# Performance work log

Hardware: AMD Instinct MI355X
Metric: run time of the kernel (lower is better)

The kernel has to match this reference:

```python
import jax, jax.numpy as jnp
import numpy as np

NODE_NUM = 2000
D_MODEL = 2048
IN_DIM = 7
OUT_DIM = 1
NODE_DIM = 40
CONV_CH = 64
SKIP_CH = 64
DEPTH = 3
ALPHA = 0.05
BATCH = 64
KERNEL = D_MODEL - NODE_NUM + 1  # 49
LN_EPS = 1e-5


def setup_inputs() -> dict:
    key = jax.random.key(0)
    ks = jax.random.split(key, 12)
    s = 0.02
    return {
        "x": jax.random.normal(ks[0], (BATCH, IN_DIM * D_MODEL), dtype=jnp.float32),
        "nodevec1": jax.random.normal(ks[1], (NODE_NUM, NODE_DIM), dtype=jnp.float32),
        "nodevec2": jax.random.normal(ks[2], (NODE_DIM, NODE_NUM), dtype=jnp.float32),
        "w_start": jax.random.normal(ks[3], (CONV_CH, IN_DIM, KERNEL), dtype=jnp.float32) * s,
        "b_start": jnp.zeros((CONV_CH,), dtype=jnp.float32),
        "w_mlp": jax.random.normal(ks[4], (SKIP_CH, (DEPTH + 1) * CONV_CH), dtype=jnp.float32) * s,
        "b_mlp": jnp.zeros((SKIP_CH,), dtype=jnp.float32),
        "w_end": jax.random.normal(ks[5], (OUT_DIM, SKIP_CH), dtype=jnp.float32) * s,
        "b_end": jnp.zeros((OUT_DIM,), dtype=jnp.float32),
        "w_lin": jax.random.normal(ks[6], (D_MODEL, NODE_NUM), dtype=jnp.float32) * s,
        "b_lin": jnp.zeros((D_MODEL,), dtype=jnp.float32),
        "ln_g": jnp.ones((D_MODEL,), dtype=jnp.float32),
        "ln_b": jnp.zeros((D_MODEL,), dtype=jnp.float32),
    }


def _conv1d(x, w, b):
    # x: (B, Cin, L), w: (Cout, Cin, K) -> (B, Cout, L-K+1)
    y = jax.lax.conv_general_dilated(x, w, window_strides=(1,), padding='VALID',
                                     dimension_numbers=('NCH', 'OIH', 'NCH'))
    return y + b[None, :, None]


def _layernorm(x, g, b):
    mu = jnp.mean(x, axis=-1, keepdims=True)
    var = jnp.mean(jnp.square(x - mu), axis=-1, keepdims=True)
    return (x - mu) * jax.lax.rsqrt(var + LN_EPS) * g + b


def reference(x, nodevec1, nodevec2, w_start, b_start, w_mlp, b_mlp,
              w_end, b_end, w_lin, b_lin, ln_g, ln_b):
    # adaptive adjacency: softmax(relu(E1 @ E2), axis=1)
    adp = jax.nn.softmax(jax.nn.relu(nodevec1 @ nodevec2), axis=1)  # (N, N)

    out = x.reshape(x.shape[0], IN_DIM, D_MODEL)
    out = _conv1d(out, w_start, b_start)  # (B, CONV_CH, N)

    # mixprop
    adj = adp + jnp.eye(NODE_NUM, dtype=adp.dtype)
    a = adj / jnp.sum(adj, axis=1, keepdims=True)  # row-normalized (N, N)
    h = out
    hops = [h]
    for _ in range(DEPTH):
        # einsum('ncw,vw->ncv', h, a)
        h = ALPHA * out + (1.0 - ALPHA) * jnp.einsum('bcw,vw->bcv', h, a)
        hops.append(h)
    ho = jnp.concatenate(hops, axis=1)  # (B, (DEPTH+1)*CONV_CH, N)
    ho = jnp.einsum('bcn,oc->bon', ho, w_mlp) + b_mlp[None, :, None]  # 1x1 conv

    out = jax.nn.gelu(ho, approximate=False)
    out = jnp.einsum('bcn,oc->bon', out, w_end) + b_end[None, :, None]  # (B, 1, N)
    out = jnp.squeeze(out, axis=1)  # (B, N)
    out = out @ w_lin.T + b_lin  # (B, D_MODEL)
    out = _layernorm(out, ln_g, ln_b)
    return out.reshape(out.shape[0], -1)
```

## Files before the change

### kernel.cpp

```cpp
#include <hip/hip_runtime.h>

#define NODE_NUM 2000
#define DM 2048
#define IN_DIM 7
#define CONV_CH 64
#define KER 49
#define BATCH 64

typedef __attribute__((ext_vector_type(8))) short bf16x8;
typedef __attribute__((ext_vector_type(4))) float f32x4;
typedef __attribute__((ext_vector_type(4))) unsigned int u32x4;

__device__ __forceinline__ float bf2f(unsigned short u) {
  union { unsigned int i; float f; } c; c.i = ((unsigned int)u) << 16; return c.f;
}
__device__ __forceinline__ unsigned short f2bf(float f) {
  union { float f; unsigned int i; } c; c.f = f;
  unsigned int r = c.i + 0x7FFFu + ((c.i >> 16) & 1u);
  return (unsigned short)(r >> 16);
}

__global__ __launch_bounds__(256) void adj_kernel(const float* __restrict__ nv1,
                                                  const float* __restrict__ nv2,
                                                  unsigned short* __restrict__ Ab) {
  const int bid = blockIdx.x;
  const int tid = threadIdx.x;
  if (bid >= 500) {
    const int r0 = 2000 + (bid - 500) * 4;
    for (int i = tid; i < 4 * 2048; i += 256)
      Ab[(size_t)(r0 + (i >> 11)) * DM + (i & 2047)] = 0;
    return;
  }
  const int v0 = bid * 4;
  __shared__ float e1s[4][40];
  __shared__ float redm[4][4], redsum[4][4];
  for (int i = tid; i < 160; i += 256) e1s[i / 40][i % 40] = nv1[(v0 + i / 40) * 40 + i % 40];
  __syncthreads();
  const int w0 = tid * 8;
  const bool oob = (w0 >= NODE_NUM);
  const float* base = nv2 + (oob ? 0 : w0);
  float acc[4][8] = {};
  f32x4 xa = *(const f32x4*)(base);
  f32x4 xb = *(const f32x4*)(base + 4);
  for (int k = 0; k < 40; ++k) {
    const f32x4 ca = xa, cb = xb;
    if (k < 39) {
      xa = *(const f32x4*)(base + (k + 1) * NODE_NUM);
      xb = *(const f32x4*)(base + (k + 1) * NODE_NUM + 4);
    }
#pragma unroll
    for (int v = 0; v < 4; ++v) {
      const float e = e1s[v][k];
#pragma unroll
      for (int i = 0; i < 4; ++i) {
        acc[v][i]     = fmaf(e, ca[i], acc[v][i]);
        acc[v][i + 4] = fmaf(e, cb[i], acc[v][i + 4]);
      }
    }
  }
  const int wid = tid >> 6, lane = tid & 63;
#pragma unroll
  for (int v = 0; v < 4; ++v) {
    float mx = -1e30f;
    if (!oob) {
#pragma unroll
      for (int i = 0; i < 8; ++i) {
        acc[v][i] = fmaxf(acc[v][i], 0.f);
        mx = fmaxf(mx, acc[v][i]);
      }
    }
    for (int o = 32; o; o >>= 1) mx = fmaxf(mx, __shfl_xor(mx, o));
    if (lane == 0) redm[v][wid] = mx;
  }
  __syncthreads();
#pragma unroll
  for (int v = 0; v < 4; ++v) {
    const float mx = fmaxf(fmaxf(redm[v][0], redm[v][1]), fmaxf(redm[v][2], redm[v][3]));
    float sum = 0.f;
    if (!oob) {
#pragma unroll
      for (int i = 0; i < 8; ++i) { const float e = __expf(acc[v][i] - mx); acc[v][i] = e; sum += e; }
    }
    for (int o = 32; o; o >>= 1) sum += __shfl_xor(sum, o);
    if (lane == 0) redsum[v][wid] = sum;
  }
  __syncthreads();
#pragma unroll
  for (int v = 0; v < 4; ++v) {
    const float sum = redsum[v][0] + redsum[v][1] + redsum[v][2] + redsum[v][3];
    const float inv = 0.5f / sum;
    const int vg = v0 + v;
    unsigned short out[8];
#pragma unroll
    for (int i = 0; i < 8; ++i) {
      const float val = oob ? 0.f : (acc[v][i] * inv + ((w0 + i == vg) ? 0.5f : 0.f));
      out[i] = f2bf(val);
    }
    *(u32x4*)(Ab + (size_t)vg * DM + w0) = *(const u32x4*)out;
  }
}

__global__ __launch_bounds__(256) void wpack_kernel(const float* __restrict__ wst,
                                                    unsigned short* __restrict__ wpack) {
  const int idx = blockIdx.x * 256 + threadIdx.x;
  const int e = idx & 7;
  const int lane = (idx >> 3) & 63;
  const int w = (idx >> 9) & 3;
  const int kstep = idx >> 11;
  const int c = w * 16 + (lane & 15);
  const int k = kstep * 32 + (lane >> 4) * 8 + e;
  const int ci = k >> 6, kern = k & 63;
  const float val = (kern < KER) ? wst[(c * IN_DIM + ci) * KER + kern] : 0.f;
  wpack[idx] = f2bf(val);
}

__global__ __launch_bounds__(256) void wmpack_kernel(const float* __restrict__ wm,
                                                     unsigned short* __restrict__ wmb) {
  const int idx = blockIdx.x * 256 + threadIdx.x;
  wmb[idx] = f2bf(wm[idx]);
}

__global__ __launch_bounds__(256) void conv_kernel(const float* __restrict__ x,
                                                   const unsigned short* __restrict__ wpack,
                                                   const float* __restrict__ bst,
                                                   unsigned short* __restrict__ H0) {
  __shared__ alignas(16) unsigned short xcopy[8 * 7 * 128];
  const int b = blockIdx.y;
  const int n0 = blockIdx.x * 64;
  const int tid = threadIdx.x;
  const int wv = tid >> 6, lane = tid & 63;
  const int l15 = lane & 15, kg = lane >> 4;
  bf16x8 af[14];
#pragma unroll
  for (int ks = 0; ks < 14; ++ks)
    af[ks] = *(const bf16x8*)(wpack + ((size_t)(ks * 4 + wv) * 64 + lane) * 8);
  f32x4 acc[4];
  {
    const f32x4 bv = *(const f32x4*)(bst + wv * 16 + kg * 4);
#pragma unroll
    for (int nf = 0; nf < 4; ++nf) acc[nf] = bv;
  }
  const size_t xb = (size_t)b * (IN_DIM * DM);
#pragma unroll
  for (int it = 0; it < 14; ++it) {
    const int row = it * 4 + (tid >> 6);
    const int s = row / 7, ci = row % 7;
    const int j = (tid & 63) * 2;
    int g0 = n0 + j + s;     if (g0 > DM - 1) g0 = DM - 1;
    int g1 = n0 + j + 1 + s; if (g1 > DM - 1) g1 = DM - 1;
    const float v0 = x[xb + ci * DM + g0];
    const float v1 = x[xb + ci * DM + g1];
    const unsigned int pk = (unsigned int)f2bf(v0) | ((unsigned int)f2bf(v1) << 16);
    *(unsigned int*)((char*)xcopy + row * 256 + j * 2) = pk;
  }
  __syncthreads();
#pragma unroll
  for (int ks = 0; ks < 14; ++ks) {
    const int ci = ks >> 1;
    const int kern0 = ((ks & 1) << 5) + kg * 8;
#pragma unroll
    for (int nf = 0; nf < 4; ++nf) {
      const int q = nf * 16 + l15 + kern0;
      const int byte = ((q & 7) * 7 + ci) * 256 + (q & ~7) * 2;
      const bf16x8 bfr = *(const bf16x8*)((const char*)xcopy + byte);
      acc[nf] = __builtin_amdgcn_mfma_f32_16x16x32_bf16(af[ks], bfr, acc[nf], 0, 0, 0);
    }
  }
#pragma unroll
  for (int nf = 0; nf < 4; ++nf) {
#pragma unroll
    for (int r = 0; r < 4; ++r) {
      const int c = wv * 16 + kg * 4 + r;
      const int n = n0 + nf * 16 + l15;
      H0[(size_t)(b * 64 + c) * DM + n] =
          (n < NODE_NUM) ? f2bf(acc[nf][r]) : (unsigned short)0;
    }
  }
}

template <int MODE>
__global__ __launch_bounds__(256) void gemm_nt(const unsigned short* __restrict__ A,
                                               const unsigned short* __restrict__ Bt,
                                               const unsigned short* __restrict__ H0,
                                               void* __restrict__ Cout) {
  __shared__ alignas(16) unsigned short As[2][128 * 64];
  __shared__ alignas(16) unsigned short Bs[2][128 * 64];
  const int tid = threadIdx.x;
  int bx, by;
  if (MODE == 0) {
    const int lin = blockIdx.y * 16 + blockIdx.x;
    const int swz = (lin & 7) * 64 + (lin >> 3);
    bx = swz & 15;  by = swz >> 4;
  } else {
    bx = blockIdx.x;  by = blockIdx.y;
  }
  const int n0 = bx * 128;
  const int m0 = (MODE == 0) ? by * 128 : 0;
  const int kbeg = (MODE == 0) ? 0 : by * 256;
  const int nt = (MODE == 0) ? (DM / 64) : 4;
  const int wid = tid >> 6, lane = tid & 63;
  const int wr = wid >> 1, wc = wid & 1;
  const int l15 = lane & 15, kg = lane >> 4;

  auto STAGE = [&](int buf, int k0) {
#pragma unroll
    for (int it = 0; it < 4; ++it) {
      const int lin = it * 4096 + tid * 16;
      const int row = lin >> 7;
      const int blog = (lin & 127) ^ ((row & 7) << 4);
      const char* sa = (const char*)A + ((size_t)(m0 + row) * DM + k0) * 2 + blog;
      const char* sb = (const char*)Bt + ((size_t)(n0 + row) * DM + k0) * 2 + blog;
      __builtin_amdgcn_global_load_lds((const __attribute__((address_space(1))) void*)sa,
                                       (__attribute__((address_space(3))) void*)((char*)As[buf] + lin),
                                       16, 0, 0);
      __builtin_amdgcn_global_load_lds((const __attribute__((address_space(1))) void*)sb,
                                       (__attribute__((address_space(3))) void*)((char*)Bs[buf] + lin),
                                       16, 0, 0);
    }
  };

  f32x4 acc[4][4] = {};
  STAGE(0, kbeg);
  STAGE(1, kbeg + 64);

  for (int t = 0; t < nt; ++t) {
    const int cur = t & 1;
    if (t + 1 < nt) asm volatile("s_waitcnt vmcnt(8)" ::: "memory");
    else            asm volatile("s_waitcnt vmcnt(0)" ::: "memory");
    __builtin_amdgcn_s_barrier();
    __builtin_amdgcn_sched_barrier(0);
    bf16x8 af[2][4], bfr[2][4];
#pragma unroll
    for (int f = 0; f < 4; ++f) {
      const int ra = wr * 64 + f * 16 + l15;
      const int rb = wc * 64 + f * 16 + l15;
#pragma unroll
      for (int kk = 0; kk < 2; ++kk) {
        const int off = kk * 64 + kg * 16;
        af[kk][f]  = *(const bf16x8*)((const char*)As[cur] + ra * 128 + (off ^ ((ra & 7) << 4)));
        bfr[kk][f] = *(const bf16x8*)((const char*)Bs[cur] + rb * 128 + (off ^ ((rb & 7) << 4)));
      }
    }
    asm volatile("s_waitcnt lgkmcnt(0)" ::: "memory");
    __builtin_amdgcn_sched_barrier(0);
    __builtin_amdgcn_s_barrier();
    __builtin_amdgcn_sched_barrier(0);
    if (t + 2 < nt) STAGE(cur, kbeg + (t + 2) * 64);
#pragma unroll
    for (int kk = 0; kk < 2; ++kk)
#pragma unroll
      for (int mf = 0; mf < 4; ++mf)
#pragma unroll
        for (int nf = 0; nf < 4; ++nf)
          acc[mf][nf] = __builtin_amdgcn_mfma_f32_16x16x32_bf16(af[kk][mf], bfr[kk][nf],
                                                                acc[mf][nf], 0, 0, 0);
  }
  const int l4 = lane >> 4;
#pragma unroll
  for (int mf = 0; mf < 4; ++mf) {
#pragma unroll
    for (int nf = 0; nf < 4; ++nf) {
#pragma unroll
      for (int r = 0; r < 4; ++r) {
        const int gm = m0 + wr * 64 + mf * 16 + l4 * 4 + r;
        const int gn = n0 + wc * 64 + nf * 16 + l15;
        if (MODE == 0) {
          const float v = 0.05f * bf2f(H0[(size_t)gm * DM + gn]) + 0.95f * acc[mf][nf][r];
          ((unsigned short*)Cout)[(size_t)gm * DM + gn] = f2bf(v);
        } else {
          if (gm < 64)
            ((float*)Cout)[(size_t)blockIdx.y * 64 * DM + (size_t)gm * DM + gn] = acc[mf][nf][r];
        }
      }
    }
  }
}

__global__ __launch_bounds__(256) void mlp_kernel(const unsigned short* __restrict__ h0,
                                                  const unsigned short* __restrict__ h1,
                                                  const unsigned short* __restrict__ h2,
                                                  const unsigned short* __restrict__ h3,
                                                  const unsigned short* __restrict__ wmb,
                                                  const float* __restrict__ bm,
                                                  const float* __restrict__ we,
                                                  const float* __restrict__ be,
                                                  unsigned short* __restrict__ out1) {
  __shared__ alignas(16) unsigned short hs[64 * 264];
  __shared__ alignas(16) unsigned short wl[64 * 264];
  __shared__ float cbuf[128];
  const int b = blockIdx.y;
  const int gn0 = blockIdx.x * 64;
  const int tid = threadIdx.x;
#pragma unroll
  for (int it = 0; it < 8; ++it) {
    const int idx = it * 256 + tid;
    const int o = idx >> 5, c = (idx & 31) * 8;
    *(bf16x8*)&wl[o * 264 + c] = *(const bf16x8*)(wmb + o * 256 + c);
  }
  if (tid < 64) cbuf[tid] = bm[tid];
  else if (tid < 128) cbuf[tid] = we[tid - 64];
  char* hsb = (char*)hs;
#pragma unroll
  for (int it = 0; it < 8; ++it) {
    const int idx = it * 256 + tid;
    const int cf = idx >> 3, n0 = (idx & 7) * 8;
    const int hop = cf >> 6, c = cf & 63;
    const unsigned short* hb = (hop == 0) ? h0 : (hop == 1) ? h1 : (hop == 2) ? h2 : h3;
    const unsigned long long* p =
        (const unsigned long long*)(hb + (size_t)(b * 64 + c) * DM + gn0 + n0);
    const unsigned long long lo = p[0], hi = p[1];
#pragma unroll
    for (int t = 0; t < 8; ++t) {
      const int i = (t + tid) & 7;
      const unsigned short val = (unsigned short)(((i & 4) ? hi : lo) >> ((i & 3) * 16));
      *(unsigned short*)(hsb + (n0 + i) * 528 + cf * 2) = val;
    }
  }
  __syncthreads();
  const int wid = tid >> 6, lane = tid & 63;
  const int l15 = lane & 15, kg = lane >> 4;
  const char* wb = (const char*)wl;
  f32x4 acc[4] = {};
#pragma unroll
  for (int kk = 0; kk < 8; ++kk) {
    const int koff = kk * 64 + kg * 16;
    const bf16x8 bfr = *(const bf16x8*)(hsb + (wid * 16 + l15) * 528 + koff);
#pragma unroll
    for (int mf = 0; mf < 4; ++mf) {
      const bf16x8 af = *(const bf16x8*)(wb + (mf * 16 + l15) * 528 + koff);
      acc[mf] = __builtin_amdgcn_mfma_f32_16x16x32_bf16(af, bfr, acc[mf], 0, 0, 0);
    }
  }
  float pl = 0.f;
#pragma unroll
  for (int mf = 0; mf < 4; ++mf) {
#pragma unroll
    for (int r = 0; r < 4; ++r) {
      const int o = mf * 16 + kg * 4 + r;
      const float s = acc[mf][r] + cbuf[o];
      const float g = 0.5f * s * (1.f + erff(s * 0.70710678118f));
      pl += cbuf[64 + o] * g;
    }
  }
  pl += __shfl_xor(pl, 16);
  pl += __shfl_xor(pl, 32);
  if (kg == 0) {
    const int n = gn0 + wid * 16 + l15;
    out1[(size_t)b * DM + n] = (n < NODE_NUM) ? f2bf(pl + be[0]) : (unsigned short)0;
  }
}

__global__ __launch_bounds__(256) void wlin_cvt(const float* __restrict__ wlin,
                                                unsigned short* __restrict__ wl) {
  const int idx = (blockIdx.x * 256 + threadIdx.x) * 8;
  const int d = idx >> 11, w0 = idx & 2047;
  unsigned short out[8];
#pragma unroll
  for (int j = 0; j < 8; ++j) {
    const int w = w0 + j;
    out[j] = (w < NODE_NUM) ? f2bf(wlin[d * NODE_NUM + w]) : (unsigned short)0;
  }
  *(u32x4*)(wl + idx) = *(const u32x4*)out;
}

__global__ __launch_bounds__(256) void ln_kernel(const float* __restrict__ yp,
                                                 const float* __restrict__ bl,
                                                 const float* __restrict__ g,
                                                 const float* __restrict__ bb,
                                                 float* __restrict__ out) {
  const int b = blockIdx.x, tid = threadIdx.x;
  __shared__ float rs[4], rq[4];
  float v[8];
  float s = 0.f;
#pragma unroll
  for (int i = 0; i < 8; ++i) {
    const int d = i * 256 + tid;
    float acc = bl[d];
#pragma unroll
    for (int sp = 0; sp < 8; ++sp) acc += yp[(size_t)sp * 64 * DM + (size_t)b * DM + d];
    v[i] = acc;
    s += acc;
  }
  for (int o = 32; o; o >>= 1) s += __shfl_xor(s, o);
  const int wid = tid >> 6, lane = tid & 63;
  if (lane == 0) rs[wid] = s;
  __syncthreads();
  s = rs[0] + rs[1] + rs[2] + rs[3];
  const float mu = s * (1.f / 2048.f);
  float q = 0.f;
#pragma unroll
  for (int i = 0; i < 8; ++i) { const float d = v[i] - mu; q += d * d; }
  for (int o = 32; o; o >>= 1) q += __shfl_xor(q, o);
  if (lane == 0) rq[wid] = q;
  __syncthreads();
  q = rq[0] + rq[1] + rq[2] + rq[3];
  const float inv = rsqrtf(q * (1.f / 2048.f) + 1e-5f);
#pragma unroll
  for (int i = 0; i < 8; ++i) {
    const int d = i * 256 + tid;
    out[(size_t)b * DM + d] = (v[i] - mu) * inv * g[d] + bb[d];
  }
}

extern "C" void kernel_launch(void* const* d_in, const int* in_sizes, int n_in,
                              void* d_out, int out_size, void* d_ws, size_t ws_size,
                              hipStream_t stream) {
  const float* x      = (const float*)d_in[0];
  const float* nv1    = (const float*)d_in[1];
  const float* nv2    = (const float*)d_in[2];
  const float* w_st   = (const float*)d_in[3];
  const float* b_st   = (const float*)d_in[4];
  const float* w_mlp  = (const float*)d_in[5];
  const float* b_mlp  = (const float*)d_in[6];
  const float* w_end  = (const float*)d_in[7];
  const float* b_end  = (const float*)d_in[8];
  const float* w_lin  = (const float*)d_in[9];
  const float* b_lin  = (const float*)d_in[10];
  const float* ln_g   = (const float*)d_in[11];
  const float* ln_b   = (const float*)d_in[12];

  char* ws = (char*)d_ws;
  const size_t SZ_A = (size_t)DM * DM * 2;
  const size_t SZ_H = (size_t)4096 * DM * 2;
  unsigned short* Ab    = (unsigned short*)(ws);
  unsigned short* H0    = (unsigned short*)(ws + SZ_A);
  unsigned short* H1    = (unsigned short*)(ws + SZ_A + SZ_H);
  unsigned short* H2    = (unsigned short*)(ws + SZ_A + 2 * SZ_H);
  unsigned short* H3    = (unsigned short*)(ws + SZ_A + 3 * SZ_H);
  unsigned short* OUT1  = (unsigned short*)(ws + SZ_A + 4 * SZ_H);
  unsigned short* WPACK = (unsigned short*)(ws + SZ_A + 4 * SZ_H + 262144);
  unsigned short* WMB   = (unsigned short*)(ws + SZ_A + 4 * SZ_H + 319488);
  unsigned short* WL    = (unsigned short*)(ws + SZ_A + 4 * SZ_H + 524288);
  float*          YP    = (float*)(ws + SZ_A + 4 * SZ_H + 524288 + SZ_A);

  wpack_kernel<<<112, 256, 0, stream>>>(w_st, WPACK);
  wmpack_kernel<<<64, 256, 0, stream>>>(w_mlp, WMB);
  adj_kernel<<<512, 256, 0, stream>>>(nv1, nv2, Ab);
  conv_kernel<<<dim3(32, BATCH), 256, 0, stream>>>(x, WPACK, b_st, H0);
  wlin_cvt<<<2048, 256, 0, stream>>>(w_lin, WL);

  gemm_nt<0><<<dim3(16, 32), 256, 0, stream>>>(H0, Ab, H0, (void*)H1);
  gemm_nt<0><<<dim3(16, 32), 256, 0, stream>>>(H1, Ab, H0, (void*)H2);
  gemm_nt<0><<<dim3(16, 32), 256, 0, stream>>>(H2, Ab, H0, (void*)H3);

  mlp_kernel<<<dim3(32, BATCH), 256, 0, stream>>>(H0, H1, H2, H3, WMB, b_mlp,
                                                  w_end, b_end, OUT1);
  gemm_nt<1><<<dim3(16, 8), 256, 0, stream>>>(OUT1, WL, (const unsigned short*)0, (void*)YP);
  ln_kernel<<<BATCH, 256, 0, stream>>>(YP, b_lin, ln_g, ln_b, (float*)d_out);
}
```

Before: 263.7 us.

## Use 256x128 tile GEMM with 512 threads and interleaved prefetch for mixprop hops

Replaces the 128x128-tile, 256-thread mixprop GEMM with a 256x128-tile, 8-wave kernel. Next-tile global-to-LDS loads are spread across the MFMA phases, and MFMA issue priority is raised. This raises reuse of the shared adjacency tile and overlaps loads with compute. The grid shrinks from 512 to 256 blocks and LDS use rises, which could lower occupancy and leave CUs idle on a 256-CU part. The tail GEMM is split into its own non-templated kernel.

```diff
diff --git a/kernel.cpp b/kernel.cpp
--- a/kernel.cpp
+++ b/kernel.cpp
@@ -178,26 +178,119 @@
   }
 }
 
-template <int MODE>
-__global__ __launch_bounds__(256) void gemm_nt(const unsigned short* __restrict__ A,
+__global__ __launch_bounds__(512) void gemm256(const unsigned short* __restrict__ A,
                                                const unsigned short* __restrict__ Bt,
                                                const unsigned short* __restrict__ H0,
-                                               void* __restrict__ Cout) {
+                                               unsigned short* __restrict__ C) {
+  __shared__ alignas(16) unsigned short As[2][256 * 64];
+  __shared__ alignas(16) unsigned short Bs[2][128 * 64];
+  const int tid = threadIdx.x;
+  const int lin = blockIdx.y * 16 + blockIdx.x;
+  const int swz = (lin & 7) * 32 + (lin >> 3);
+  const int bx = swz & 15, by = swz >> 4;
+  const int n0 = bx * 128, m0 = by * 256;
+  const int wid = tid >> 6, lane = tid & 63;
+  const int wr = wid >> 2, wc = wid & 3;
+  const int l15 = lane & 15, kg = lane >> 4;
+
+  auto stageA = [&](int buf, int k0, int it) {
+    const int linb = it * 8192 + tid * 16;
+    const int row = linb >> 7;
+    const int blog = (linb & 127) ^ ((row & 7) << 4);
+    const char* s = (const char*)A + ((size_t)(m0 + row) * DM + k0) * 2 + blog;
+    __builtin_amdgcn_global_load_lds((const __attribute__((address_space(1))) void*)s,
+        (__attribute__((address_space(3))) void*)((char*)As[buf] + linb), 16, 0, 0);
+  };
+  auto stageB = [&](int buf, int k0, int it) {
+    const int linb = it * 8192 + tid * 16;
+    const int row = linb >> 7;
+    const int blog = (linb & 127) ^ ((row & 7) << 4);
+    const char* s = (const char*)Bt + ((size_t)(n0 + row) * DM + k0) * 2 + blog;
+    __builtin_amdgcn_global_load_lds((const __attribute__((address_space(1))) void*)s,
+        (__attribute__((address_space(3))) void*)((char*)Bs[buf] + linb), 16, 0, 0);
+  };
+
+  f32x4 acc[8][2] = {};
+  stageA(0, 0, 0); stageA(0, 0, 1); stageA(0, 0, 2); stageA(0, 0, 3);
+  stageB(0, 0, 0); stageB(0, 0, 1);
+
+  for (int t = 0; t < 32; ++t) {
+    const int cur = t & 1, nxt = cur ^ 1;
+    const int kn = (t + 1) * 64;
+    const bool pf = (t + 1 < 32);
+    asm volatile("s_waitcnt vmcnt(0)" ::: "memory");
+    __builtin_amdgcn_s_barrier();
+    __builtin_amdgcn_sched_barrier(0);
+    bf16x8 bfrag[2][2];
+#pragma unroll
+    for (int p = 0; p < 4; ++p) {
+      bf16x8 afr[2][2];
+#pragma unroll
+      for (int ml = 0; ml < 2; ++ml) {
+        const int ra = wr * 128 + (p * 2 + ml) * 16 + l15;
+        const int rowoff = ra * 128;
+        const int sw = (ra & 7) << 4;
+#pragma unroll
+        for (int kk = 0; kk < 2; ++kk)
+          afr[kk][ml] = *(const bf16x8*)((const char*)As[cur] + rowoff + ((kk * 64 + kg * 16) ^ sw));
+      }
+      if (p == 0) {
+#pragma unroll
+        for (int nf = 0; nf < 2; ++nf) {
+          const int rb = wc * 32 + nf * 16 + l15;
+          const int rowoff = rb * 128;
+          const int sw = (rb & 7) << 4;
+#pragma unroll
+          for (int kk = 0; kk < 2; ++kk)
+            bfrag[kk][nf] = *(const bf16x8*)((const char*)Bs[cur] + rowoff + ((kk * 64 + kg * 16) ^ sw));
+        }
+      }
+      if (pf) {
+        if (p == 0) { stageA(nxt, kn, 0); stageA(nxt, kn, 1); }
+        else if (p == 1) { stageA(nxt, kn, 2); stageA(nxt, kn, 3); }
+        else if (p == 2) { stageB(nxt, kn, 0); stageB(nxt, kn, 1); }
+      }
+      asm volatile("s_waitcnt lgkmcnt(0)" ::: "memory");
+      __builtin_amdgcn_sched_barrier(0);
+      __builtin_amdgcn_s_setprio(1);
+#pragma unroll
+      for (int kk = 0; kk < 2; ++kk)
+#pragma unroll
+        for (int ml = 0; ml < 2; ++ml)
+#pragma unroll
+          for (int nf = 0; nf < 2; ++nf)
+            acc[p * 2 + ml][nf] = __builtin_amdgcn_mfma_f32_16x16x32_bf16(
+                afr[kk][ml], bfrag[kk][nf], acc[p * 2 + ml][nf], 0, 0, 0);
+      __builtin_amdgcn_s_setprio(0);
+    }
+  }
+  const int l4 = lane >> 4;
+#pragma unroll
+  for (int mf = 0; mf < 8; ++mf) {
+#pragma unroll
+    for (int nf = 0; nf < 2; ++nf) {
+#pragma unroll
+      for (int r = 0; r < 4; ++r) {
+        const int gm = m0 + wr * 128 + mf * 16 + l4 * 4 + r;
+        const int gn = n0 + wc * 32 + nf * 16 + l15;
+        const float v = 0.05f * bf2f(H0[(size_t)gm * DM + gn]) + 0.95f * acc[mf][nf][r];
+        C[(size_t)gm * DM + gn] = f2bf(v);
+      }
+    }
+  }
+}
+
+__global__ __launch_bounds__(256) void gemm_tail(const unsigned short* __restrict__ A,
+                                                 const unsigned short* __restrict__ Bt,
+                                                 float* __restrict__ Cout) {
   __shared__ alignas(16) unsigned short As[2][128 * 64];
   __shared__ alignas(16) unsigned short Bs[2][128 * 64];
   const int tid = threadIdx.x;
-  int bx, by;
-  if (MODE == 0) {
-    const int lin = blockIdx.y * 16 + blockIdx.x;
-    const int swz = (lin & 7) * 64 + (lin >> 3);
-    bx = swz & 15;  by = swz >> 4;
-  } else {
-    bx = blockIdx.x;  by = blockIdx.y;
-  }
+  const int bx = blockIdx.x, by = blockIdx.y;
   const int n0 = bx * 128;
-  const int m0 = (MODE == 0) ? by * 128 : 0;
-  const int kbeg = (MODE == 0) ? 0 : by * 256;
-  const int nt = (MODE == 0) ? (DM / 64) : 4;
+  const int m0 = 0;
+  const int kbeg = by * 256;
+  const int nt = 4;
   const int wid = tid >> 6, lane = tid & 63;
   const int wr = wid >> 1, wc = wid & 1;
   const int l15 = lane & 15, kg = lane >> 4;
@@ -264,13 +357,8 @@
       for (int r = 0; r < 4; ++r) {
         const int gm = m0 + wr * 64 + mf * 16 + l4 * 4 + r;
         const int gn = n0 + wc * 64 + nf * 16 + l15;
-        if (MODE == 0) {
-          const float v = 0.05f * bf2f(H0[(size_t)gm * DM + gn]) + 0.95f * acc[mf][nf][r];
-          ((unsigned short*)Cout)[(size_t)gm * DM + gn] = f2bf(v);
-        } else {
-          if (gm < 64)
-            ((float*)Cout)[(size_t)blockIdx.y * 64 * DM + (size_t)gm * DM + gn] = acc[mf][nf][r];
-        }
+        if (gm < 64)
+          Cout[(size_t)by * 64 * DM + (size_t)gm * DM + gn] = acc[mf][nf][r];
       }
     }
   }
@@ -439,12 +527,12 @@
   conv_kernel<<<dim3(32, BATCH), 256, 0, stream>>>(x, WPACK, b_st, H0);
   wlin_cvt<<<2048, 256, 0, stream>>>(w_lin, WL);
 
-  gemm_nt<0><<<dim3(16, 32), 256, 0, stream>>>(H0, Ab, H0, (void*)H1);
-  gemm_nt<0><<<dim3(16, 32), 256, 0, stream>>>(H1, Ab, H0, (void*)H2);
-  gemm_nt<0><<<dim3(16, 32), 256, 0, stream>>>(H2, Ab, H0, (void*)H3);
+  gemm256<<<dim3(16, 16), 512, 0, stream>>>(H0, Ab, H0, H1);
+  gemm256<<<dim3(16, 16), 512, 0, stream>>>(H1, Ab, H0, H2);
+  gemm256<<<dim3(16, 16), 512, 0, stream>>>(H2, Ab, H0, H3);
 
   mlp_kernel<<<dim3(32, BATCH), 256, 0, stream>>>(H0, H1, H2, H3, WMB, b_mlp,
                                                   w_end, b_end, OUT1);
-  gemm_nt<1><<<dim3(16, 8), 256, 0, stream>>>(OUT1, WL, (const unsigned short*)0, (void*)YP);
+  gemm_tail<<<dim3(16, 8), 256, 0, stream>>>(OUT1, WL, YP);
   ln_kernel<<<BATCH, 256, 0, stream>>>(YP, b_lin, ln_g, ln_b, (float*)d_out);
 }
```

Result: slower. 306.7 us (+16.3%).
